# Kernel tuning notes

Measured on AMD Instinct MI355X. Metric: run time of the kernel, lower is better.

Reference implementation:

```python
import jax, jax.numpy as jnp
import numpy as np

T, B, C = 512, 64, 512
ALPHA = 0.6        # blend coefficient from __init__
TAU = 10.0         # LIF tau
VTH = 1.0          # LIF v_threshold (v_reset = 0, hard reset)
BN_EPS = 1e-5


def spike_fn(x):
    # forward heaviside: spike = (v - v_th >= 0)
    return (x >= 0.0).astype(x.dtype)


def setup_inputs() -> dict:
    key = jax.random.key(0)
    ks = jax.random.split(key, 7)
    x = jax.random.normal(ks[0], (T, B, C), dtype=jnp.float32)
    conv_w = jax.random.normal(ks[1], (C, C, 3), dtype=jnp.float32) / np.sqrt(3.0 * C)
    conv_b = jax.random.normal(ks[2], (C,), dtype=jnp.float32) * 0.01
    bn_gamma = 0.5 + jax.random.uniform(ks[3], (C,), dtype=jnp.float32)
    bn_beta = jax.random.normal(ks[4], (C,), dtype=jnp.float32) * 0.1
    bn_mean = jax.random.normal(ks[5], (C,), dtype=jnp.float32) * 0.1
    bn_var = 0.5 + jax.random.uniform(ks[6], (C,), dtype=jnp.float32)
    return {"x": x, "conv_w": conv_w, "conv_b": conv_b,
            "bn_gamma": bn_gamma, "bn_beta": bn_beta,
            "bn_mean": bn_mean, "bn_var": bn_var}


def reference(x, conv_w, conv_b, bn_gamma, bn_beta, bn_mean, bn_var):
    # x: (T, B, C). Conv1d(k=3, pad=1) on a length-1 sequence reduces to a
    # dense matmul with the middle kernel tap: out = prev @ w[:,:,1].T + b.
    w1 = conv_w[:, :, 1]                      # (C_out, C_in)
    inv_std = bn_gamma * jax.lax.rsqrt(bn_var + BN_EPS)   # fused BN scale
    Bsz, Csz = x.shape[1], x.shape[2]

    def step(carry, x_t):
        prev, v = carry                        # prev: (B, C), v: (B, C) membrane
        conv = jnp.einsum('bc,dc->bd', prev, w1) + conv_b
        bn = (conv - bn_mean) * inv_std + bn_beta
        # LIF (decay_input=True, v_reset=0): v += (x - v) / tau
        v = v + (bn - v) / TAU
        s = spike_fn(v - VTH)
        v = v * (1.0 - s)                      # hard reset to 0
        new = (1.0 - ALPHA) * x_t + ALPHA * s  # alpha blend
        return (new, v), new                   # prev_state detached in torch; no-op for fwd

    init = (jnp.zeros((Bsz, Csz), x.dtype), jnp.zeros((Bsz, Csz), x.dtype))
    _, out = jax.lax.scan(step, init, x)       # out: (T, B, C)
    return out
```

## Files before the change

kernel.cpp:

```cpp
#include <hip/hip_runtime.h>
#include <stdint.h>

#define T_STEPS 512
#define BATCH 64
#define CH 512

using short8 = __attribute__((ext_vector_type(8))) short;
using f32x4  = __attribute__((ext_vector_type(4))) float;

__device__ __forceinline__ unsigned short f2b(float f) {
    union { float f; unsigned u; } c; c.f = f;
    unsigned r = (c.u + 0x7FFFu + ((c.u >> 16) & 1u)) >> 16;
    return (unsigned short)r;
}
__device__ __forceinline__ float b2f(unsigned short h) {
    union { unsigned u; float f; } c; c.u = ((unsigned)h) << 16;
    return c.f;
}

__device__ __forceinline__ void gload_lds16(const void* g, void* l) {
    __builtin_amdgcn_global_load_lds(
        (__attribute__((address_space(1))) unsigned int*)(g),
        (__attribute__((address_space(3))) unsigned int*)(l),
        16, 0, 0);
}

__global__ void prep(const float* __restrict__ cw, const float* __restrict__ cb,
                     const float* __restrict__ gamma, const float* __restrict__ beta,
                     const float* __restrict__ mean, const float* __restrict__ var,
                     unsigned short* __restrict__ wb,
                     float* __restrict__ wt,
                     float* __restrict__ isb,
                     float* __restrict__ k0p,
                     int* __restrict__ flag) {
    int idx = blockIdx.x * 256 + threadIdx.x;
    if (idx == 0) *flag = 0x7fffffff;
    if (idx >= CH * CH) return;
    int d = idx >> 9, c = idx & 511;
    float is = gamma[d] * rsqrtf(var[d] + 1e-5f);
    float w = cw[((size_t)d * CH + c) * 3 + 1];
    int ksb = c >> 5, kq4 = (c >> 3) & 3, e = c & 7;
    wb[(size_t)ksb * 16384 + (kq4 * 512 + d) * 8 + e] = f2b(0.04f * is * w);
    wt[(size_t)c * CH + d] = w;
    if (c == 0) {
        isb[d] = is;
        k0p[d] = 0.1f * ((cb[d] - mean[d]) * is + beta[d]);
    }
}

#define GBM 128
#define GBK 32
#define PADK 40

__global__ __launch_bounds__(512, 2) void gemm_fused(
    const float* __restrict__ Xp,
    const unsigned short* __restrict__ wbp,
    const float* __restrict__ k0p,
    unsigned short* __restrict__ Wbuf,
    float* __restrict__ outp,
    int Mc)
{
    __shared__ __align__(16) unsigned short As[2][GBM][PADK];
    __shared__ __align__(16) unsigned short Bs[2][4][512][8];
    int tid = threadIdx.x;
    int lane = tid & 63, wid = tid >> 6;
    int wm = wid >> 2, wn = wid & 3;
    int i0 = blockIdx.x * GBM;
    int fm = lane & 15, fq = lane >> 4;
    int kq = fq * 8;

    int ar = tid >> 2;
    int ac = (tid & 3) * 8;

    float b0e[8];
    #pragma unroll
    for (int j = 0; j < 8; ++j) b0e[j] = k0p[wn * 128 + j * 16 + fm];

    f32x4 acc[4][8] = {};

    int grow = i0 + ar;
    bool arv = grow < Mc;
    int growc = arv ? grow : (Mc - 1);
    const float* xrow = &Xp[(size_t)growc * CH];
    float* orow = &outp[(size_t)grow * CH];

    const char* gBw = (const char*)wbp + wid * 4096 + lane * 16;
    char* lBw = (char*)Bs + wid * 4096;

    {
        #pragma unroll
        for (int q = 0; q < 4; ++q)
            gload_lds16(gBw + q * 1024, lBw + q * 1024);
        float4 a0 = *(const float4*)&xrow[ac];
        float4 a1 = *(const float4*)&xrow[ac + 4];
        short8 av;
        av[0]=f2b(a0.x); av[1]=f2b(a0.y); av[2]=f2b(a0.z); av[3]=f2b(a0.w);
        av[4]=f2b(a1.x); av[5]=f2b(a1.y); av[6]=f2b(a1.z); av[7]=f2b(a1.w);
        *(short8*)&As[0][ar][ac] = av;
        if (arv) {
            *(float4*)&orow[ac]     = make_float4(0.4f*a0.x, 0.4f*a0.y, 0.4f*a0.z, 0.4f*a0.w);
            *(float4*)&orow[ac + 4] = make_float4(0.4f*a1.x, 0.4f*a1.y, 0.4f*a1.z, 0.4f*a1.w);
        }
    }
    __syncthreads();

    for (int ks = 0; ks < 16; ++ks) {
        int cur = ks & 1;
        int kn = (ks + 1) * GBK;
        float4 na0, na1;
        if (kn < 512) {
            const char* g = gBw + (size_t)(ks + 1) * 32768;
            char* l = lBw + (cur ^ 1) * 32768;
            #pragma unroll
            for (int q = 0; q < 4; ++q)
                gload_lds16(g + q * 1024, l + q * 1024);
            na0 = *(const float4*)&xrow[kn + ac];
            na1 = *(const float4*)&xrow[kn + ac + 4];
        }
        short8 af[4], bfr[8];
        #pragma unroll
        for (int i = 0; i < 4; ++i)
            af[i] = *(const short8*)&As[cur][wm * 64 + i * 16 + fm][kq];
        const short8* bb = (const short8*)((const char*)Bs + cur * 32768 + fq * 8192);
        #pragma unroll
        for (int j = 0; j < 8; ++j)
            bfr[j] = bb[wn * 128 + j * 16 + fm];
        #pragma unroll
        for (int i = 0; i < 4; ++i)
            #pragma unroll
            for (int j = 0; j < 8; ++j)
                acc[i][j] = __builtin_amdgcn_mfma_f32_16x16x32_bf16(af[i], bfr[j], acc[i][j], 0, 0, 0);
        if (kn < 512) {
            short8 av;
            av[0]=f2b(na0.x); av[1]=f2b(na0.y); av[2]=f2b(na0.z); av[3]=f2b(na0.w);
            av[4]=f2b(na1.x); av[5]=f2b(na1.y); av[6]=f2b(na1.z); av[7]=f2b(na1.w);
            *(short8*)&As[cur ^ 1][ar][ac] = av;
            if (arv) {
                *(float4*)&orow[kn + ac]     = make_float4(0.4f*na0.x, 0.4f*na0.y, 0.4f*na0.z, 0.4f*na0.w);
                *(float4*)&orow[kn + ac + 4] = make_float4(0.4f*na1.x, 0.4f*na1.y, 0.4f*na1.z, 0.4f*na1.w);
            }
        }
        __syncthreads();
    }

    #pragma unroll
    for (int i = 0; i < 4; ++i)
        #pragma unroll
        for (int r = 0; r < 4; ++r) {
            int row = i0 + wm * 64 + i * 16 + fq * 4 + r;
            if (row < Mc) {
                #pragma unroll
                for (int j = 0; j < 8; ++j) {
                    int col = wn * 128 + j * 16 + fm;
                    Wbuf[(size_t)row * CH + col] = f2b(acc[i][j][r] + b0e[j]);
                }
            }
        }
}

__device__ __forceinline__ short8 wload(const unsigned short* Wbuf, int t, int a0, int b, int c0) {
    int r = t - 1 - a0; if (r < 0) r = 0;
    return *(const short8*)&Wbuf[((size_t)r * BATCH + b) * CH + c0];
}

__global__ __launch_bounds__(64) void scan_a(
    const unsigned short* __restrict__ Wbuf,
    const float* __restrict__ k0p,
    float* __restrict__ Sbuf,
    int t0, int a0, int segs)
{
    int b = blockIdx.x & (BATCH - 1);
    int seg = blockIdx.x >> 6;
    int lane = threadIdx.x, c0 = lane * 8;
    int tstart = t0 + seg * 64;

    float B0[8];
    #pragma unroll
    for (int k = 0; k < 8; ++k) B0[k] = k0p[c0 + k];

    float S[8] = {};
    short8 pz[8];
    #pragma unroll
    for (int p = 0; p < 8; ++p) pz[p] = wload(Wbuf, tstart + p, a0, b, c0);

    for (int ii = 0; ii < 64; ii += 8) {
        #pragma unroll
        for (int p = 0; p < 8; ++p) {
            int t = tstart + ii + p;
            short8 zv = pz[p];
            int tn = ii + p + 8;
            if (tn < 64) pz[p] = wload(Wbuf, tstart + tn, a0, b, c0);
            #pragma unroll
            for (int k = 0; k < 8; ++k) {
                float wv = (t == 0) ? B0[k] : b2f((unsigned short)zv[k]);
                S[k] = fmaf(0.9f, S[k], wv);
            }
        }
    }
    float* sp = &Sbuf[((size_t)b * segs + seg) * CH + c0];
    *(float4*)&sp[0] = make_float4(S[0], S[1], S[2], S[3]);
    *(float4*)&sp[4] = make_float4(S[4], S[5], S[6], S[7]);
}

__global__ __launch_bounds__(64) void scan_c(
    const unsigned short* __restrict__ Wbuf,
    const float* __restrict__ k0p,
    const float* __restrict__ Sbuf,
    const float* __restrict__ vcin,
    float* __restrict__ vcout,
    int* __restrict__ flag,
    int t0, int a0, int segs, int chunk_idx)
{
    const float F = 1.1790184577738595e-3f;
    int b = blockIdx.x & (BATCH - 1);
    int seg = blockIdx.x >> 6;
    int lane = threadIdx.x, c0 = lane * 8;
    int tstart = t0 + seg * 64;

    float B0[8];
    #pragma unroll
    for (int k = 0; k < 8; ++k) B0[k] = k0p[c0 + k];

    float v[8];
    if (t0 == 0) {
        #pragma unroll
        for (int k = 0; k < 8; ++k) v[k] = 0.0f;
    } else {
        const float* vp = &vcin[(size_t)b * CH + c0];
        float4 v0 = *(const float4*)&vp[0], v1 = *(const float4*)&vp[4];
        v[0]=v0.x; v[1]=v0.y; v[2]=v0.z; v[3]=v0.w; v[4]=v1.x; v[5]=v1.y; v[6]=v1.z; v[7]=v1.w;
    }
    for (int u = 0; u < seg; ++u) {
        const float* sp = &Sbuf[((size_t)b * segs + u) * CH + c0];
        float4 s0 = *(const float4*)&sp[0], s1 = *(const float4*)&sp[4];
        float sv[8] = {s0.x, s0.y, s0.z, s0.w, s1.x, s1.y, s1.z, s1.w};
        #pragma unroll
        for (int k = 0; k < 8; ++k) v[k] = fmaf(v[k], F, sv[k]);
    }

    bool anyhit = false;
    short8 pz[8];
    #pragma unroll
    for (int p = 0; p < 8; ++p) pz[p] = wload(Wbuf, tstart + p, a0, b, c0);

    for (int ii = 0; ii < 64; ii += 8) {
        #pragma unroll
        for (int p = 0; p < 8; ++p) {
            int t = tstart + ii + p;
            short8 zv = pz[p];
            int tn = ii + p + 8;
            if (tn < 64) pz[p] = wload(Wbuf, tstart + tn, a0, b, c0);
            float m = -1e30f;
            #pragma unroll
            for (int k = 0; k < 8; ++k) {
                float wv = (t == 0) ? B0[k] : b2f((unsigned short)zv[k]);
                v[k] = fmaf(0.9f, v[k], wv);
                m = fmaxf(m, v[k]);
            }
            anyhit |= (m >= 0.995f);
        }
    }
    if (__ballot(anyhit) != 0ULL && lane == 0) atomicMin(flag, chunk_idx);
    if (seg == segs - 1) {
        float* vp = &vcout[(size_t)b * CH + c0];
        *(float4*)&vp[0] = make_float4(v[0], v[1], v[2], v[3]);
        *(float4*)&vp[4] = make_float4(v[4], v[5], v[6], v[7]);
    }
}

__global__ __launch_bounds__(64) void seq_fix(
    const float* __restrict__ x,
    const float* __restrict__ wt,
    const unsigned short* __restrict__ Wbuf,
    const float* __restrict__ isb,
    const float* __restrict__ k0p,
    const int* __restrict__ flag,
    const float* __restrict__ vcin,
    float* __restrict__ out,
    float* __restrict__ v_state,
    unsigned long long* __restrict__ s_state,
    int t0, int t1, int a0, int chunk_idx, int save_state)
{
    int fl = *flag;
    if (fl > chunk_idx) return;
    int b = blockIdx.x;
    int lane = threadIdx.x;
    int c0 = lane * 8;

    float is6[8], B0[8];
    #pragma unroll
    for (int k = 0; k < 8; ++k) {
        is6[k] = 0.06f * isb[c0 + k];
        B0[k]  = k0p[c0 + k];
    }

    float v[8];
    unsigned long long mk[8];
    if (t0 == 0) {
        #pragma unroll
        for (int k = 0; k < 8; ++k) v[k] = 0.0f;
        #pragma unroll
        for (int j = 0; j < 8; ++j) mk[j] = 0ULL;
    } else if (fl == chunk_idx) {
        #pragma unroll
        for (int k = 0; k < 8; ++k) v[k] = vcin[(size_t)b * CH + c0 + k];
        #pragma unroll
        for (int j = 0; j < 8; ++j) mk[j] = 0ULL;
    } else {
        #pragma unroll
        for (int k = 0; k < 8; ++k) v[k] = v_state[(size_t)b * CH + c0 + k];
        #pragma unroll
        for (int j = 0; j < 8; ++j) mk[j] = s_state[b * 8 + j];
    }

    float xc[8]; short8 wc;
    {
        const float4* xp = (const float4*)&x[((size_t)t0 * BATCH + b) * CH + c0];
        float4 x0 = xp[0], x1 = xp[1];
        xc[0]=x0.x; xc[1]=x0.y; xc[2]=x0.z; xc[3]=x0.w; xc[4]=x1.x; xc[5]=x1.y; xc[6]=x1.z; xc[7]=x1.w;
        wc = wload(Wbuf, t0, a0, b, c0);
    }
    for (int t = t0; t < t1; ++t) {
        float xn[8]; short8 wn_;
        if (t + 1 < t1) {
            const float4* xp = (const float4*)&x[((size_t)(t + 1) * BATCH + b) * CH + c0];
            float4 x0 = xp[0], x1 = xp[1];
            xn[0]=x0.x; xn[1]=x0.y; xn[2]=x0.z; xn[3]=x0.w; xn[4]=x1.x; xn[5]=x1.y; xn[6]=x1.z; xn[7]=x1.w;
            wn_ = wload(Wbuf, t + 1, a0, b, c0);
        }
        float acc[8] = {};
        unsigned long long anym = mk[0]|mk[1]|mk[2]|mk[3]|mk[4]|mk[5]|mk[6]|mk[7];
        if (anym) {
            #pragma unroll
            for (int j = 0; j < 8; ++j) {
                unsigned long long m = mk[j];
                while (m) {
                    int l = __builtin_ctzll(m); m &= m - 1;
                    const float4* wr = (const float4*)&wt[(size_t)(l * 8 + j) * CH + c0];
                    float4 w0 = wr[0], w1 = wr[1];
                    acc[0]+=w0.x; acc[1]+=w0.y; acc[2]+=w0.z; acc[3]+=w0.w;
                    acc[4]+=w1.x; acc[5]+=w1.y; acc[6]+=w1.z; acc[7]+=w1.w;
                }
            }
        }
        bool s[8];
        #pragma unroll
        for (int k = 0; k < 8; ++k) {
            float wv = (t == 0) ? B0[k] : b2f((unsigned short)wc[k]);
            float vv = fmaf(0.9f, v[k], fmaf(is6[k], acc[k], wv));
            s[k] = (vv >= 1.0f);
            v[k] = s[k] ? 0.0f : vv;
        }
        float4* op = (float4*)&out[((size_t)t * BATCH + b) * CH + c0];
        op[0] = make_float4(fmaf(0.4f,xc[0],s[0]?0.6f:0.f), fmaf(0.4f,xc[1],s[1]?0.6f:0.f),
                            fmaf(0.4f,xc[2],s[2]?0.6f:0.f), fmaf(0.4f,xc[3],s[3]?0.6f:0.f));
        op[1] = make_float4(fmaf(0.4f,xc[4],s[4]?0.6f:0.f), fmaf(0.4f,xc[5],s[5]?0.6f:0.f),
                            fmaf(0.4f,xc[6],s[6]?0.6f:0.f), fmaf(0.4f,xc[7],s[7]?0.6f:0.f));
        #pragma unroll
        for (int j = 0; j < 8; ++j) mk[j] = __ballot(s[j]);
        #pragma unroll
        for (int k = 0; k < 8; ++k) xc[k] = xn[k];
        wc = wn_;
    }
    if (save_state) {
        #pragma unroll
        for (int k = 0; k < 8; ++k) v_state[(size_t)b * CH + c0 + k] = v[k];
        if (lane < 8) s_state[b * 8 + lane] = mk[lane];
    }
}

extern "C" void kernel_launch(void* const* d_in, const int* in_sizes, int n_in,
                              void* d_out, int out_size, void* d_ws, size_t ws_size,
                              hipStream_t stream) {
    const float* x     = (const float*)d_in[0];
    const float* cw    = (const float*)d_in[1];
    const float* cb    = (const float*)d_in[2];
    const float* gamma = (const float*)d_in[3];
    const float* beta  = (const float*)d_in[4];
    const float* mean  = (const float*)d_in[5];
    const float* var   = (const float*)d_in[6];
    float* out = (float*)d_out;

    char* ws = (char*)d_ws;
    size_t off = 0;
    auto alloc = [&](size_t bytes) -> char* {
        char* p = ws + off;
        off = (off + bytes + 255) & ~(size_t)255;
        return p;
    };
    unsigned short* wb = (unsigned short*)alloc((size_t)CH * CH * 2);
    float* wt  = (float*)alloc((size_t)CH * CH * 4);
    float* isb = (float*)alloc(CH * 4);
    float* k0p = (float*)alloc(CH * 4);
    int* flag  = (int*)alloc(256);
    float* vst = (float*)alloc((size_t)BATCH * CH * 4);
    unsigned long long* sst = (unsigned long long*)alloc(BATCH * 8 * 8);
    float* vca = (float*)alloc((size_t)BATCH * CH * 4);
    float* vcb = (float*)alloc((size_t)BATCH * CH * 4);
    float* Sb  = (float*)alloc((size_t)BATCH * 8 * CH * 4);
    unsigned short* Wbuf = (unsigned short*)(ws + off);

    size_t avail = (ws_size > off) ? ws_size - off : 0;
    long rows = (long)(avail / ((size_t)BATCH * CH * 2));
    long cs = ((rows - 1) / 64) * 64;
    if (cs > T_STEPS) cs = T_STEPS;
    if (cs < 64) cs = 64;
    int CS = (int)cs;

    hipLaunchKernelGGL(prep, dim3((CH * CH + 255) / 256), dim3(256), 0, stream,
                       cw, cb, gamma, beta, mean, var, wb, wt, isb, k0p, flag);

    float *vin = vca, *vout = vcb;
    int k = 0;
    for (int t0 = 0; t0 < T_STEPS; t0 += CS, ++k) {
        int t1 = t0 + CS; if (t1 > T_STEPS) t1 = T_STEPS;
        int a0 = (t0 == 0) ? 0 : t0 - 1;
        int gend = (t1 == T_STEPS) ? T_STEPS : t1 - 1;
        int Mc = (gend - a0) * BATCH;
        hipLaunchKernelGGL(gemm_fused, dim3((Mc + GBM - 1) / GBM), dim3(512), 0, stream,
                           x + (size_t)a0 * BATCH * CH, wb, k0p, Wbuf,
                           out + (size_t)a0 * BATCH * CH, Mc);
        int segs = (t1 - t0) / 64;
        hipLaunchKernelGGL(scan_a, dim3(BATCH * segs), dim3(64), 0, stream,
                           Wbuf, k0p, Sb, t0, a0, segs);
        hipLaunchKernelGGL(scan_c, dim3(BATCH * segs), dim3(64), 0, stream,
                           Wbuf, k0p, Sb, vin, vout, flag, t0, a0, segs, k);
        hipLaunchKernelGGL(seq_fix, dim3(BATCH), dim3(64), 0, stream,
                           x, wt, Wbuf, isb, k0p, flag, vin, out, vst, sst,
                           t0, t1, a0, k, (t1 < T_STEPS) ? 1 : 0);
        float* tmp = vin; vin = vout; vout = tmp;
    }
}
```

Before: 72.13 us.

## Stream fp32 A tiles into swizzled LDS via direct global-to-LDS loads

The X tile is now loaded as fp32 straight into LDS with global_load_lds, using an XOR swizzle to avoid bank conflicts, instead of being loaded into registers, converted to bf16 and stored. The bf16 conversion moves to fragment-read time, and the 0.4*x output is written from LDS. The goal is to cut register staging and VGPR pressure and to overlap A loads asynchronously. In exchange the A tile uses twice the LDS and each wave redoes the conversion work. f2b now calls the library __float2bfloat16.

```diff
diff --git a/kernel.cpp b/kernel.cpp
--- a/kernel.cpp
+++ b/kernel.cpp
@@ -1,4 +1,5 @@
 #include <hip/hip_runtime.h>
+#include <hip/hip_bf16.h>
 #include <stdint.h>
 
 #define T_STEPS 512
@@ -9,9 +10,9 @@
 using f32x4  = __attribute__((ext_vector_type(4))) float;
 
 __device__ __forceinline__ unsigned short f2b(float f) {
-    union { float f; unsigned u; } c; c.f = f;
-    unsigned r = (c.u + 0x7FFFu + ((c.u >> 16) & 1u)) >> 16;
-    return (unsigned short)r;
+    union { __hip_bfloat16 h; unsigned short u; } c;
+    c.h = __float2bfloat16(f);
+    return c.u;
 }
 __device__ __forceinline__ float b2f(unsigned short h) {
     union { unsigned u; float f; } c; c.u = ((unsigned)h) << 16;
@@ -50,7 +51,6 @@
 
 #define GBM 128
 #define GBK 32
-#define PADK 40
 
 __global__ __launch_bounds__(512, 2) void gemm_fused(
     const float* __restrict__ Xp,
@@ -60,17 +60,13 @@
     float* __restrict__ outp,
     int Mc)
 {
-    __shared__ __align__(16) unsigned short As[2][GBM][PADK];
+    __shared__ __align__(16) float As[2][GBM][GBK];
     __shared__ __align__(16) unsigned short Bs[2][4][512][8];
     int tid = threadIdx.x;
     int lane = tid & 63, wid = tid >> 6;
     int wm = wid >> 2, wn = wid & 3;
     int i0 = blockIdx.x * GBM;
     int fm = lane & 15, fq = lane >> 4;
-    int kq = fq * 8;
-
-    int ar = tid >> 2;
-    int ac = (tid & 3) * 8;
 
     float b0e[8];
     #pragma unroll
@@ -78,49 +74,66 @@
 
     f32x4 acc[4][8] = {};
 
-    int grow = i0 + ar;
-    bool arv = grow < Mc;
-    int growc = arv ? grow : (Mc - 1);
-    const float* xrow = &Xp[(size_t)growc * CH];
-    float* orow = &outp[(size_t)grow * CH];
-
+    const float* xsrc[2];
+    float* odst[2];
+    bool valid[2];
+    #pragma unroll
+    for (int q = 0; q < 2; ++q) {
+        int row = q * 64 + (tid >> 3);
+        int inner = (tid & 7) * 16;
+        int innerS = inner ^ ((row & 7) << 4);
+        int grow = i0 + row;
+        valid[q] = grow < Mc;
+        int gc = valid[q] ? grow : (Mc - 1);
+        xsrc[q] = &Xp[(size_t)gc * CH + (innerS >> 2)];
+        odst[q] = &outp[(size_t)grow * CH + (innerS >> 2)];
+    }
     const char* gBw = (const char*)wbp + wid * 4096 + lane * 16;
-    char* lBw = (char*)Bs + wid * 4096;
 
     {
         #pragma unroll
         for (int q = 0; q < 4; ++q)
-            gload_lds16(gBw + q * 1024, lBw + q * 1024);
-        float4 a0 = *(const float4*)&xrow[ac];
-        float4 a1 = *(const float4*)&xrow[ac + 4];
-        short8 av;
-        av[0]=f2b(a0.x); av[1]=f2b(a0.y); av[2]=f2b(a0.z); av[3]=f2b(a0.w);
-        av[4]=f2b(a1.x); av[5]=f2b(a1.y); av[6]=f2b(a1.z); av[7]=f2b(a1.w);
-        *(short8*)&As[0][ar][ac] = av;
-        if (arv) {
-            *(float4*)&orow[ac]     = make_float4(0.4f*a0.x, 0.4f*a0.y, 0.4f*a0.z, 0.4f*a0.w);
-            *(float4*)&orow[ac + 4] = make_float4(0.4f*a1.x, 0.4f*a1.y, 0.4f*a1.z, 0.4f*a1.w);
-        }
+            gload_lds16(gBw + q * 1024, (char*)Bs + wid * 4096 + q * 1024);
+        #pragma unroll
+        for (int q = 0; q < 2; ++q)
+            gload_lds16(xsrc[q], (char*)As + q * 8192 + tid * 16);
     }
     __syncthreads();
 
     for (int ks = 0; ks < 16; ++ks) {
         int cur = ks & 1;
-        int kn = (ks + 1) * GBK;
-        float4 na0, na1;
-        if (kn < 512) {
+        if (ks + 1 < 16) {
             const char* g = gBw + (size_t)(ks + 1) * 32768;
-            char* l = lBw + (cur ^ 1) * 32768;
+            char* lB = (char*)Bs + (cur ^ 1) * 32768 + wid * 4096;
             #pragma unroll
             for (int q = 0; q < 4; ++q)
-                gload_lds16(g + q * 1024, l + q * 1024);
-            na0 = *(const float4*)&xrow[kn + ac];
-            na1 = *(const float4*)&xrow[kn + ac + 4];
+                gload_lds16(g + q * 1024, lB + q * 1024);
+            char* lA = (char*)As + (cur ^ 1) * 16384 + tid * 16;
+            #pragma unroll
+            for (int q = 0; q < 2; ++q)
+                gload_lds16(xsrc[q] + (ks + 1) * 32, lA + q * 8192);
+        }
+        #pragma unroll
+        for (int q = 0; q < 2; ++q) {
+            if (valid[q]) {
+                const f32x4 v = *(const f32x4*)((const char*)As + cur * 16384 + q * 8192 + tid * 16);
+                f32x4 o = {0.4f * v[0], 0.4f * v[1], 0.4f * v[2], 0.4f * v[3]};
+                *(f32x4*)(odst[q] + ks * 32) = o;
+            }
         }
         short8 af[4], bfr[8];
         #pragma unroll
-        for (int i = 0; i < 4; ++i)
-            af[i] = *(const short8*)&As[cur][wm * 64 + i * 16 + fm][kq];
+        for (int i = 0; i < 4; ++i) {
+            int r = wm * 64 + i * 16 + fm;
+            int s = (r & 7) << 4;
+            const char* abase = (const char*)As + cur * 16384 + r * 128;
+            f32x4 lo = *(const f32x4*)(abase + ((fq * 32) ^ s));
+            f32x4 hi = *(const f32x4*)(abase + ((fq * 32 + 16) ^ s));
+            short8 av;
+            av[0]=f2b(lo[0]); av[1]=f2b(lo[1]); av[2]=f2b(lo[2]); av[3]=f2b(lo[3]);
+            av[4]=f2b(hi[0]); av[5]=f2b(hi[1]); av[6]=f2b(hi[2]); av[7]=f2b(hi[3]);
+            af[i] = av;
+        }
         const short8* bb = (const short8*)((const char*)Bs + cur * 32768 + fq * 8192);
         #pragma unroll
         for (int j = 0; j < 8; ++j)
@@ -130,16 +143,6 @@
             #pragma unroll
             for (int j = 0; j < 8; ++j)
                 acc[i][j] = __builtin_amdgcn_mfma_f32_16x16x32_bf16(af[i], bfr[j], acc[i][j], 0, 0, 0);
-        if (kn < 512) {
-            short8 av;
-            av[0]=f2b(na0.x); av[1]=f2b(na0.y); av[2]=f2b(na0.z); av[3]=f2b(na0.w);
-            av[4]=f2b(na1.x); av[5]=f2b(na1.y); av[6]=f2b(na1.z); av[7]=f2b(na1.w);
-            *(short8*)&As[cur ^ 1][ar][ac] = av;
-            if (arv) {
-                *(float4*)&orow[kn + ac]     = make_float4(0.4f*na0.x, 0.4f*na0.y, 0.4f*na0.z, 0.4f*na0.w);
-                *(float4*)&orow[kn + ac + 4] = make_float4(0.4f*na1.x, 0.4f*na1.y, 0.4f*na1.z, 0.4f*na1.w);
-            }
-        }
         __syncthreads();
     }
 
```

Result: faster. 68.37 us (-5.2%).
